# Performance work log

Hardware: AMD Instinct MI355X
Metric: run time of the kernel (lower is better)

## Reference

```python
import math
import jax, jax.numpy as jnp
import numpy as np

B, L, D, H = 2, 2048, 2048, 32
HD = D // H  # 64
ROPE_BASE = 10000.0


def _rope_tables():
    # standard RoPE: angles [L, HD/2], duplicated to [L, HD]
    inv_freq = 1.0 / (ROPE_BASE ** (np.arange(0, HD, 2, dtype=np.float32) / HD))
    t = np.arange(L, dtype=np.float32)
    ang = np.outer(t, inv_freq)                      # [L, HD/2]
    emb = np.concatenate([ang, ang], axis=-1)        # [L, HD]
    cos = np.broadcast_to(np.cos(emb), (B, L, HD)).copy()
    sin = np.broadcast_to(np.sin(emb), (B, L, HD)).copy()
    return jnp.asarray(cos), jnp.asarray(sin)


def setup_inputs() -> dict:
    key = jax.random.key(0)
    kx, kq, kp = jax.random.split(key, 3)
    x = jax.random.normal(kx, (B, L, D), dtype=jnp.float32)
    Wqkv = jax.random.normal(kq, (3 * D, D), dtype=jnp.float32) * 0.02
    Wproj = jax.random.normal(kp, (D, D), dtype=jnp.float32) * 0.02
    cos, sin = _rope_tables()
    return {"x": x, "cos": cos, "sin": sin, "Wqkv": Wqkv, "Wproj": Wproj}


def _rotate_half(t):
    t1, t2 = jnp.split(t, 2, axis=-1)
    return jnp.concatenate([-t2, t1], axis=-1)


def reference(x, cos, sin, Wqkv, Wproj):
    # fused QKV projection: [B,L,3D]
    qkv = jnp.einsum('bld,ed->ble', x, Wqkv)
    qkv = qkv.reshape(B, L, 3, H, HD).transpose(2, 0, 3, 1, 4)  # [3,B,H,L,HD]
    q, k, v = qkv[0], qkv[1], qkv[2]
    # RoPE (cos/sin broadcast over heads, matching cos.unsqueeze(1))
    c = cos[:, None, :, :]  # [B,1,L,HD]
    s = sin[:, None, :, :]
    q = q * c + _rotate_half(q) * s
    k = k * c + _rotate_half(k) * s
    # causal SDPA (L > 1 -> is_causal=True)
    scores = jnp.einsum('bhqd,bhkd->bhqk', q, k) / math.sqrt(HD)
    causal = jnp.tril(jnp.ones((L, L), dtype=bool))
    scores = jnp.where(causal, scores, jnp.float32(-1e30))
    attn = jax.nn.softmax(scores, axis=-1)
    y = jnp.einsum('bhqk,bhkd->bhqd', attn, v)
    y = y.transpose(0, 2, 1, 3).reshape(B, L, D)
    return jnp.einsum('bld,ed->ble', y, Wproj)
```

## Files before the change

### kernel.cpp

```cpp
#include <hip/hip_runtime.h>
#include <stdint.h>

#define DEV static __device__ __forceinline__

typedef __attribute__((ext_vector_type(8))) short bf16x8;
typedef __attribute__((ext_vector_type(4))) float f32x4;

DEV unsigned short f2b(float f){
  union { float f; unsigned int u; } v; v.f = f;
  return (unsigned short)((v.u + 0x7FFFu + ((v.u >> 16) & 1u)) >> 16);
}

#define SWZ(v, pat) __int_as_float(__builtin_amdgcn_ds_swizzle(__float_as_int(v), pat))

#define GLD16(g, l) __builtin_amdgcn_global_load_lds(                         \
    (const __attribute__((address_space(1))) void*)(g),                       \
    (__attribute__((address_space(3))) void*)(l), 16, 0, 0)

#define BAR() do { asm volatile("" ::: "memory"); __builtin_amdgcn_s_barrier(); \
                   asm volatile("" ::: "memory"); } while(0)

__global__ __launch_bounds__(256) void cvt_all(const float* __restrict__ a,
                                               const float* __restrict__ b,
                                               const float* __restrict__ c,
                                               unsigned short* __restrict__ oa,
                                               unsigned short* __restrict__ ob,
                                               unsigned short* __restrict__ oc){
  const int n1 = 2097152, n2 = 3145728, n3 = 1048576;
  int stride = gridDim.x * blockDim.x;
  for (int i = blockIdx.x * blockDim.x + threadIdx.x; i < n1 + n2 + n3; i += stride){
    const float* src; unsigned short* dst; int k;
    if (i < n1)            { src = a; dst = oa; k = i; }
    else if (i < n1 + n2)  { src = b; dst = ob; k = i - n1; }
    else                   { src = c; dst = oc; k = i - n1 - n2; }
    float4 v = ((const float4*)src)[k];
    ((ushort4*)dst)[k] = make_ushort4(f2b(v.x), f2b(v.y), f2b(v.z), f2b(v.w));
  }
}

template<int MODE>
__global__ __launch_bounds__(512, 2) void gemm_r3(
    const unsigned short* __restrict__ A,
    const unsigned short* __restrict__ Bw,
    int nbn,
    const float* __restrict__ cosp, const float* __restrict__ sinp,
    unsigned short* __restrict__ Qo, unsigned short* __restrict__ Ko,
    unsigned short* __restrict__ Vo, float* __restrict__ Cout, int N)
{
  constexpr int BUF = 49152;
  __shared__ __align__(16) unsigned char lds[3 * BUF];

  const int t = threadIdx.x;
  const int wid = t >> 6, lane = t & 63;
  const int l15 = lane & 15, l4 = lane >> 4;
  const int wr = wid >> 1, wc = wid & 1;

  const int cpx = gridDim.x >> 3;
  const int bid = (blockIdx.x & 7) * cpx + (blockIdx.x >> 3);
  const int bm = bid / nbn, bn = bid % nbn;
  const int m0 = bm * 256, n0 = bn * 128;

  const int rsub = lane >> 3;
  const int sch  = (lane & 7) ^ rsub;

  auto stage = [&](int kt, int rb){
    unsigned char* base = lds + rb * BUF;
    const unsigned short* As = A + (size_t)(m0 + wid * 32 + rsub) * 2048 + kt * 64 + sch * 8;
    #pragma unroll
    for (int i = 0; i < 4; ++i)
      GLD16(As + (size_t)i * 8 * 2048, base + wid * 4096 + i * 1024);
    #pragma unroll
    for (int j = 0; j < 2; ++j){
      int rv = n0 + wid * 16 + j * 8 + rsub;
      GLD16(Bw + (size_t)rv * 2048 + kt * 64 + sch * 8, base + 32768 + wid * 2048 + j * 1024);
    }
  };

  f32x4 acc[4][4];
  #pragma unroll
  for (int mi = 0; mi < 4; ++mi)
    #pragma unroll
    for (int ni = 0; ni < 4; ++ni)
      acc[mi][ni] = (f32x4){0.f, 0.f, 0.f, 0.f};

  auto compute = [&](int rb){
    const unsigned char* Ab = lds + rb * BUF;
    const unsigned char* Bb = Ab + 32768;
    bf16x8 af[4][2], bf[4][2];
    #pragma unroll
    for (int mi = 0; mi < 4; ++mi)
      #pragma unroll
      for (int ks = 0; ks < 2; ++ks){
        int r = wr * 64 + mi * 16 + l15, ch = ks * 4 + l4;
        af[mi][ks] = *(const bf16x8*)(Ab + r * 128 + ((ch * 16) ^ ((r & 7) << 4)));
      }
    #pragma unroll
    for (int ni = 0; ni < 4; ++ni)
      #pragma unroll
      for (int ks = 0; ks < 2; ++ks){
        int r = wc * 64 + ni * 16 + l15, ch = ks * 4 + l4;
        bf[ni][ks] = *(const bf16x8*)(Bb + r * 128 + ((ch * 16) ^ ((r & 7) << 4)));
      }
    #pragma unroll
    for (int ks = 0; ks < 2; ++ks)
      #pragma unroll
      for (int mi = 0; mi < 4; ++mi)
        #pragma unroll
        for (int ni = 0; ni < 4; ++ni)
          acc[mi][ni] = __builtin_amdgcn_mfma_f32_16x16x32_bf16(af[mi][ks], bf[ni][ks], acc[mi][ni], 0, 0, 0);
  };

  stage(0, 0);
  stage(1, 1);
  asm volatile("s_waitcnt vmcnt(6)" ::: "memory");
  __builtin_amdgcn_s_barrier();
  asm volatile("" ::: "memory");

  #pragma unroll 3
  for (int kt = 0; kt < 30; ++kt){
    stage(kt + 2, (kt + 2) % 3);
    asm volatile("s_waitcnt vmcnt(12)" ::: "memory");
    compute(kt % 3);
    asm volatile("" ::: "memory");
    __builtin_amdgcn_s_barrier();
    asm volatile("" ::: "memory");
  }
  asm volatile("s_waitcnt vmcnt(6)" ::: "memory");
  compute(0);
  asm volatile("" ::: "memory");
  __builtin_amdgcn_s_barrier();
  asm volatile("" ::: "memory");
  asm volatile("s_waitcnt vmcnt(0)" ::: "memory");
  compute(1);

  if (MODE == 1){
    #pragma unroll
    for (int mi = 0; mi < 4; ++mi)
      #pragma unroll
      for (int ni = 0; ni < 4; ++ni)
        #pragma unroll
        for (int j = 0; j < 4; ++j){
          int m = m0 + wr * 64 + mi * 16 + l4 * 4 + j;
          int n = n0 + wc * 64 + ni * 16 + l15;
          Cout[(size_t)m * N + n] = acc[mi][ni][j];
        }
  } else {
    #pragma unroll
    for (int ni = 0; ni < 4; ++ni){
      int e = n0 + wc * 64 + ni * 16 + l15;
      int which = e >> 11;
      int h = (e >> 6) & 31;
      int d = e & 63;
      unsigned short* dst = (which == 0) ? Qo : (which == 1) ? Ko : Vo;
      #pragma unroll
      for (int mi = 0; mi < 4; ++mi)
        #pragma unroll
        for (int j = 0; j < 4; ++j){
          int m = m0 + wr * 64 + mi * 16 + l4 * 4 + j;
          int b = m >> 11, l = m & 2047;
          float v = acc[mi][ni][j];
          float outv;
          if (which == 2){
            outv = v;
          } else {
            float pv = acc[mi][ni ^ 2][j];
            size_t ci = (size_t)(b * 2048 + l) * 64 + d;
            outv = v * cosp[ci] + ((d < 32) ? -pv : pv) * sinp[ci];
            if (which == 0) outv *= 0.125f;
          }
          dst[(size_t)((b * 32 + h) * 2048 + l) * 64 + d] = f2b(outv);
        }
    }
  }
}

__global__ __launch_bounds__(256) void transpose_v(const unsigned short* __restrict__ V,
                                                   unsigned short* __restrict__ Vt){
  __shared__ unsigned short tile[64][72];
  int bh = blockIdx.x >> 5;
  int l0 = (blockIdx.x & 31) * 64;
  int t = threadIdx.x;
  #pragma unroll
  for (int i = 0; i < 2; ++i){
    int c = i * 256 + t;
    int row = c >> 3, ch = c & 7;
    uint4 v = *(const uint4*)(V + ((size_t)bh * 2048 + l0 + row) * 64 + ch * 8);
    const unsigned short* p = (const unsigned short*)&v;
    #pragma unroll
    for (int k = 0; k < 8; ++k) tile[row][ch * 8 + k] = p[k];
  }
  __syncthreads();
  #pragma unroll
  for (int i = 0; i < 2; ++i){
    int c = i * 256 + t;
    int drow = c >> 3, ch = c & 7;
    unsigned short tmp[8];
    #pragma unroll
    for (int k = 0; k < 8; ++k) tmp[k] = tile[ch * 8 + k][drow];
    *(uint4*)(Vt + ((size_t)bh * 64 + drow) * 2048 + l0 + ch * 8) = *(const uint4*)tmp;
  }
}

__global__ __launch_bounds__(256, 3) void attn_fwd(
    const unsigned short* __restrict__ Q, const unsigned short* __restrict__ K,
    const unsigned short* __restrict__ Vt, unsigned short* __restrict__ Y)
{
  __shared__ __align__(16) unsigned char kvb[2][16384];
  __shared__ __align__(16) unsigned char plds[4][4096];
  int idx = blockIdx.x;
  int bh = idx >> 3;
  int pr = idx & 7;
  int b = bh >> 5, h = bh & 31;
  int t = threadIdx.x, wid = t >> 6, lane = t & 63;
  int l15 = lane & 15, l4 = lane >> 4;
  const unsigned short* Qb = Q  + (size_t)bh * 2048 * 64;
  const unsigned short* Kb = K  + (size_t)bh * 2048 * 64;
  const unsigned short* Vb = Vt + (size_t)bh * 64 * 2048;
  unsigned char* myp = plds[wid];

  int srow = t >> 3;
  int sch  = (t & 7) ^ (srow & 7);

  auto stageKV = [&](int kt, int ib){
    int kv0 = kt * 64;
    unsigned char* d = kvb[ib];
    GLD16(Kb + (size_t)(kv0 + srow)      * 64   + sch * 8, d + t * 16);
    GLD16(Kb + (size_t)(kv0 + srow + 32) * 64   + sch * 8, d + 4096  + t * 16);
    GLD16(Vb + (size_t)srow        * 2048 + kv0 + sch * 8, d + 8192  + t * 16);
    GLD16(Vb + (size_t)(srow + 32) * 2048 + kv0 + sch * 8, d + 12288 + t * 16);
  };

  for (int half = 0; half < 2; ++half){
    int qt = half ? (15 - pr) : pr;
    int q0 = qt * 128 + wid * 32;

    bf16x8 aq[2][2];
    #pragma unroll
    for (int mi = 0; mi < 2; ++mi)
      #pragma unroll
      for (int ks = 0; ks < 2; ++ks)
        aq[mi][ks] = *(const bf16x8*)(Qb + (size_t)(q0 + mi * 16 + l15) * 64 + ks * 32 + l4 * 8);

    f32x4 acc[2][4];
    float ps[2][4];
    #pragma unroll
    for (int mi = 0; mi < 2; ++mi){
      #pragma unroll
      for (int nd = 0; nd < 4; ++nd) acc[mi][nd] = (f32x4){0.f, 0.f, 0.f, 0.f};
      #pragma unroll
      for (int j = 0; j < 4; ++j) ps[mi][j] = 0.f;
    }

    int my_nkt = ((q0 + 31) >> 6) + 1;
    int nb = 2 * qt + 2;

    stageKV(0, 0);
    #pragma unroll 1
    for (int kt = 0; kt < nb; ++kt){
      int ib = kt & 1;
      if (kt + 1 < nb){
        stageKV(kt + 1, ib ^ 1);
        asm volatile("s_waitcnt vmcnt(4)" ::: "memory");
      } else {
        asm volatile("s_waitcnt vmcnt(0)" ::: "memory");
      }
      BAR();
      if (kt < my_nkt){
        const unsigned char* kb = kvb[ib];
        const unsigned char* vb = kvb[ib] + 8192;
        int kv0 = kt * 64;
        bf16x8 bk[2][4];
        #pragma unroll
        for (int ks = 0; ks < 2; ++ks)
          #pragma unroll
          for (int ni = 0; ni < 4; ++ni){
            int r = ni * 16 + l15, ch = ks * 4 + l4;
            bk[ks][ni] = *(const bf16x8*)(kb + r * 128 + ((ch * 16) ^ ((r & 7) << 4)));
          }
        f32x4 s[2][4];
        #pragma unroll
        for (int mi = 0; mi < 2; ++mi)
          #pragma unroll
          for (int ni = 0; ni < 4; ++ni)
            s[mi][ni] = (f32x4){0.f, 0.f, 0.f, 0.f};
        #pragma unroll
        for (int ks = 0; ks < 2; ++ks)
          #pragma unroll
          for (int mi = 0; mi < 2; ++mi)
            #pragma unroll
            for (int ni = 0; ni < 4; ++ni)
              s[mi][ni] = __builtin_amdgcn_mfma_f32_16x16x32_bf16(aq[mi][ks], bk[ks][ni], s[mi][ni], 0, 0, 0);
        if (kt == my_nkt - 1){
          #pragma unroll
          for (int mi = 0; mi < 2; ++mi)
            #pragma unroll
            for (int ni = 0; ni < 4; ++ni)
              #pragma unroll
              for (int j = 0; j < 4; ++j){
                int kv = kv0 + ni * 16 + l15;
                int q  = q0 + mi * 16 + l4 * 4 + j;
                if (kv > q) s[mi][ni][j] = -1e30f;
              }
        }
        #pragma unroll
        for (int mi = 0; mi < 2; ++mi)
          #pragma unroll
          for (int ni = 0; ni < 4; ++ni)
            #pragma unroll
            for (int j = 0; j < 4; ++j){
              float p = __expf(s[mi][ni][j]);
              s[mi][ni][j] = p;
              ps[mi][j] += p;
            }
        #pragma unroll
        for (int mi = 0; mi < 2; ++mi)
          #pragma unroll
          for (int j = 0; j < 4; ++j){
            int r = mi * 16 + l4 * 4 + j;
            int sw = (r & 7) << 4;
            unsigned char* rowp = myp + r * 128;
            #pragma unroll
            for (int p2 = 0; p2 < 2; ++p2){
              unsigned int pk;
              asm("v_cvt_pk_bf16_f32 %0, %1, %2" : "=v"(pk) : "v"(s[mi][2 * p2][j]), "v"(s[mi][2 * p2 + 1][j]));
              *(unsigned short*)(rowp + ((p2 * 64      + 2 * l15) ^ sw)) = (unsigned short)pk;
              *(unsigned short*)(rowp + ((p2 * 64 + 32 + 2 * l15) ^ sw)) = (unsigned short)(pk >> 16);
            }
          }
        __threadfence_block();
        #pragma unroll
        for (int ks2 = 0; ks2 < 2; ++ks2){
          bf16x8 ap[2], bv[4];
          #pragma unroll
          for (int mi = 0; mi < 2; ++mi){
            int r = mi * 16 + l15;
            ap[mi] = *(const bf16x8*)(myp + r * 128 + ((ks2 * 64 + l4 * 16) ^ ((r & 7) << 4)));
          }
          #pragma unroll
          for (int nd = 0; nd < 4; ++nd){
            int r = nd * 16 + l15, ch = ks2 * 4 + l4;
            bv[nd] = *(const bf16x8*)(vb + r * 128 + ((ch * 16) ^ ((r & 7) << 4)));
          }
          #pragma unroll
          for (int mi = 0; mi < 2; ++mi)
            #pragma unroll
            for (int nd = 0; nd < 4; ++nd)
              acc[mi][nd] = __builtin_amdgcn_mfma_f32_16x16x32_bf16(ap[mi], bv[nd], acc[mi][nd], 0, 0, 0);
        }
      }
      BAR();
    }

    float lrow[2][4];
    #pragma unroll
    for (int mi = 0; mi < 2; ++mi)
      #pragma unroll
      for (int j = 0; j < 4; ++j){
        float v = ps[mi][j];
        v += SWZ(v, 0x041F);
        v += SWZ(v, 0x081F);
        v += SWZ(v, 0x101F);
        v += SWZ(v, 0x201F);
        lrow[mi][j] = v;
      }
    #pragma unroll
    for (int mi = 0; mi < 2; ++mi){
      float inv[4];
      #pragma unroll
      for (int j = 0; j < 4; ++j) inv[j] = 1.f / lrow[mi][j];
      #pragma unroll
      for (int nd = 0; nd < 4; ++nd)
        #pragma unroll
        for (int j = 0; j < 4; ++j){
          int q = q0 + mi * 16 + l4 * 4 + j;
          int d = nd * 16 + l15;
          Y[(size_t)(b * 2048 + q) * 2048 + h * 64 + d] = f2b(acc[mi][nd][j] * inv[j]);
        }
    }
  }
}

extern "C" void kernel_launch(void* const* d_in, const int* in_sizes, int n_in,
                              void* d_out, int out_size, void* d_ws, size_t ws_size,
                              hipStream_t stream){
  (void)in_sizes; (void)n_in; (void)out_size; (void)ws_size;
  const float* x     = (const float*)d_in[0];
  const float* cosp  = (const float*)d_in[1];
  const float* sinp  = (const float*)d_in[2];
  const float* Wqkv  = (const float*)d_in[3];
  const float* Wproj = (const float*)d_in[4];
  float* out = (float*)d_out;
  char* ws = (char*)d_ws;

  unsigned short* Xb  = (unsigned short*)(ws);
  unsigned short* Wqb = (unsigned short*)(ws + 16777216);
  unsigned short* Wpb = (unsigned short*)(ws + 41943040);
  unsigned short* Qb  = (unsigned short*)(ws + 50331648);
  unsigned short* Kb  = (unsigned short*)(ws + 67108864);
  unsigned short* Vb  = (unsigned short*)(ws + 83886080);
  unsigned short* Vtb = Xb;
  unsigned short* Yb  = Vb;

  cvt_all<<<2048, 256, 0, stream>>>(x, Wqkv, Wproj, Xb, Wqb, Wpb);

  gemm_r3<0><<<768, 512, 0, stream>>>(Xb, Wqb, 48, cosp, sinp, Qb, Kb, Vb, nullptr, 0);
  transpose_v<<<2048, 256, 0, stream>>>(Vb, Vtb);
  attn_fwd<<<512, 256, 0, stream>>>(Qb, Kb, Vtb, Yb);
  gemm_r3<1><<<256, 512, 0, stream>>>(Yb, Wpb, 16, nullptr, nullptr, nullptr, nullptr, nullptr, out, 2048);
}
```

Baseline: 259.4 us.

## Add dedicated QKV GEMM with 256x192 tiles and interleaved RoPE row permutation

Replaces the templated QKV projection GEMM with a new kernel that uses 256x192 output tiles (512 blocks instead of 768), double-buffered LDS with staggered A/B staging, and an 8-way sub-phased MFMA schedule with barriers and setprio. The B rows are permuted so each RoPE pair lands in adjacent lanes, letting the epilogue fetch the partner value with a ds_swizzle instead of holding it in another accumulator tile. The aim is a larger tile with more reuse per LDS load and a better fit of blocks to CUs, at the cost of more LDS per block, many extra barriers and more complex indexing. The output projection keeps the old kernel minus the template.

```diff
diff --git a/kernel.cpp b/kernel.cpp
--- a/kernel.cpp
+++ b/kernel.cpp
@@ -38,14 +38,151 @@
   }
 }
 
-template<int MODE>
+__global__ __launch_bounds__(512, 2) void gemm_8p2(
+    const unsigned short* __restrict__ A,
+    const unsigned short* __restrict__ Bw,
+    const float* __restrict__ cosp, const float* __restrict__ sinp,
+    unsigned short* __restrict__ Qo, unsigned short* __restrict__ Ko,
+    unsigned short* __restrict__ Vo)
+{
+  constexpr int BUFSZ = 57344;
+  __shared__ __align__(16) unsigned char lds[2 * BUFSZ];
+  const int t = threadIdx.x;
+  const int wid = t >> 6, lane = t & 63;
+  const int l15 = lane & 15, l4 = lane >> 4;
+  const int wr = wid >> 2, wc = wid & 3;
+  const int nbn = 32;
+  const int cpx = gridDim.x >> 3;
+  const int bid = (blockIdx.x & 7) * cpx + (blockIdx.x >> 3);
+  const int bm = bid / nbn, bn = bid % nbn;
+  const int m0 = bm * 256, n0 = bn * 192;
+
+  const int tr  = t >> 3;
+  const int sch = (t & 7) ^ (tr & 7);
+  const int trp = (tr >> 1) | ((tr & 1) << 5);
+  const unsigned short* Abase = A  + (size_t)(m0 + tr)  * 2048 + sch * 8;
+  const unsigned short* Bbase = Bw + (size_t)(n0 + trp) * 2048 + sch * 8;
+
+  auto stageA = [&](int kt, int b){
+    size_t ko = (size_t)(kt & 31) * 64;
+    unsigned char* d = lds + b * BUFSZ + t * 16;
+    GLD16(Abase + ko,                      d);
+    GLD16(Abase + (size_t) 64 * 2048 + ko, d + 8192);
+    GLD16(Abase + (size_t)128 * 2048 + ko, d + 16384);
+    GLD16(Abase + (size_t)192 * 2048 + ko, d + 24576);
+  };
+  auto stageB = [&](int kt, int b){
+    size_t ko = (size_t)(kt & 31) * 64;
+    unsigned char* d = lds + b * BUFSZ + 32768 + t * 16;
+    GLD16(Bbase + ko,                      d);
+    GLD16(Bbase + (size_t) 64 * 2048 + ko, d + 8192);
+    GLD16(Bbase + (size_t)128 * 2048 + ko, d + 16384);
+  };
+
+  auto ldA = [&](bf16x8 (&af)[4], int b, int qm, int ks){
+    const unsigned char* Ar = lds + b * BUFSZ;
+    #pragma unroll
+    for (int mi = 0; mi < 4; ++mi){
+      int rr = wr * 128 + qm * 64 + mi * 16 + l15, ch = ks * 4 + l4;
+      af[mi] = *(const bf16x8*)(Ar + rr * 128 + ((ch * 16) ^ ((rr & 7) << 4)));
+    }
+  };
+  auto ldB = [&](bf16x8 (&bq)[3], int b, int ks){
+    const unsigned char* Br = lds + b * BUFSZ + 32768;
+    #pragma unroll
+    for (int ni = 0; ni < 3; ++ni){
+      int rr = wc * 48 + ni * 16 + l15, ch = ks * 4 + l4;
+      bq[ni] = *(const bf16x8*)(Br + rr * 128 + ((ch * 16) ^ ((rr & 7) << 4)));
+    }
+  };
+
+  f32x4 acc[8][3];
+  #pragma unroll
+  for (int mi = 0; mi < 8; ++mi)
+    #pragma unroll
+    for (int ni = 0; ni < 3; ++ni)
+      acc[mi][ni] = (f32x4){0.f, 0.f, 0.f, 0.f};
+
+#define MM3(AF, BQ, QM) do {                                                  \
+    __builtin_amdgcn_s_setprio(1);                                            \
+    _Pragma("unroll")                                                         \
+    for (int mi = 0; mi < 4; ++mi)                                            \
+      _Pragma("unroll")                                                       \
+      for (int ni = 0; ni < 3; ++ni)                                          \
+        acc[(QM)*4+mi][ni] = __builtin_amdgcn_mfma_f32_16x16x32_bf16(         \
+            (AF)[mi], (BQ)[ni], acc[(QM)*4+mi][ni], 0, 0, 0);                 \
+    __builtin_amdgcn_s_setprio(0);                                            \
+  } while (0)
+
+  stageA(0, 0); stageB(0, 0); stageB(1, 1);
+  asm volatile("s_waitcnt vmcnt(3)");
+  __builtin_amdgcn_s_barrier();
+
+  bf16x8 af[4], bq[3];
+  #pragma unroll 1
+  for (int T = 0; T < 32; ++T){
+    int b = T & 1;
+    ldA(af, b, 0, 0); ldB(bq, b, 0);
+    stageA(T + 1, b ^ 1);
+    __builtin_amdgcn_s_barrier();
+    asm volatile("s_waitcnt lgkmcnt(0)");
+    MM3(af, bq, 0);
+    __builtin_amdgcn_s_barrier();
+    ldA(af, b, 1, 0);
+    __builtin_amdgcn_s_barrier();
+    asm volatile("s_waitcnt lgkmcnt(0)");
+    MM3(af, bq, 1);
+    __builtin_amdgcn_s_barrier();
+    ldA(af, b, 0, 1); ldB(bq, b, 1);
+    __builtin_amdgcn_s_barrier();
+    asm volatile("s_waitcnt lgkmcnt(0)");
+    MM3(af, bq, 0);
+    __builtin_amdgcn_s_barrier();
+    ldA(af, b, 1, 1);
+    stageB(T + 2, b);
+    asm volatile("s_waitcnt vmcnt(3)");
+    __builtin_amdgcn_s_barrier();
+    asm volatile("s_waitcnt lgkmcnt(0)");
+    MM3(af, bq, 1);
+    __builtin_amdgcn_s_barrier();
+  }
+#undef MM3
+  asm volatile("s_waitcnt vmcnt(0)");
+  __builtin_amdgcn_s_barrier();
+
+  #pragma unroll
+  for (int ni = 0; ni < 3; ++ni){
+    int e16 = n0 + wc * 48 + ni * 16;
+    int which = e16 >> 11;
+    int h = (e16 >> 6) & 31;
+    unsigned short* dst = (which == 0) ? Qo : (which == 1) ? Ko : Vo;
+    int p = (e16 & 63) + l15;
+    int d = (p >> 1) | ((p & 1) << 5);
+    #pragma unroll
+    for (int mi = 0; mi < 8; ++mi)
+      #pragma unroll
+      for (int j = 0; j < 4; ++j){
+        int m = m0 + wr * 128 + mi * 16 + l4 * 4 + j;
+        int bb = m >> 11, l = m & 2047;
+        float val = acc[mi][ni][j];
+        float par = SWZ(val, 0x041F);
+        float outv;
+        if (which == 2){
+          outv = val;
+        } else {
+          size_t ci = (size_t)(bb * 2048 + l) * 64 + d;
+          outv = val * cosp[ci] + ((p & 1) ? par : -par) * sinp[ci];
+          if (which == 0) outv *= 0.125f;
+        }
+        dst[(size_t)((bb * 32 + h) * 2048 + l) * 64 + d] = f2b(outv);
+      }
+  }
+}
+
 __global__ __launch_bounds__(512, 2) void gemm_r3(
     const unsigned short* __restrict__ A,
     const unsigned short* __restrict__ Bw,
-    int nbn,
-    const float* __restrict__ cosp, const float* __restrict__ sinp,
-    unsigned short* __restrict__ Qo, unsigned short* __restrict__ Ko,
-    unsigned short* __restrict__ Vo, float* __restrict__ Cout, int N)
+    int nbn, float* __restrict__ Cout, int N)
 {
   constexpr int BUF = 49152;
   __shared__ __align__(16) unsigned char lds[3 * BUF];
@@ -133,45 +270,16 @@
   asm volatile("s_waitcnt vmcnt(0)" ::: "memory");
   compute(1);
 
-  if (MODE == 1){
-    #pragma unroll
-    for (int mi = 0; mi < 4; ++mi)
-      #pragma unroll
-      for (int ni = 0; ni < 4; ++ni)
-        #pragma unroll
-        for (int j = 0; j < 4; ++j){
-          int m = m0 + wr * 64 + mi * 16 + l4 * 4 + j;
-          int n = n0 + wc * 64 + ni * 16 + l15;
-          Cout[(size_t)m * N + n] = acc[mi][ni][j];
-        }
-  } else {
-    #pragma unroll
-    for (int ni = 0; ni < 4; ++ni){
-      int e = n0 + wc * 64 + ni * 16 + l15;
-      int which = e >> 11;
-      int h = (e >> 6) & 31;
-      int d = e & 63;
-      unsigned short* dst = (which == 0) ? Qo : (which == 1) ? Ko : Vo;
-      #pragma unroll
-      for (int mi = 0; mi < 4; ++mi)
-        #pragma unroll
-        for (int j = 0; j < 4; ++j){
-          int m = m0 + wr * 64 + mi * 16 + l4 * 4 + j;
-          int b = m >> 11, l = m & 2047;
-          float v = acc[mi][ni][j];
-          float outv;
-          if (which == 2){
-            outv = v;
-          } else {
-            float pv = acc[mi][ni ^ 2][j];
-            size_t ci = (size_t)(b * 2048 + l) * 64 + d;
-            outv = v * cosp[ci] + ((d < 32) ? -pv : pv) * sinp[ci];
-            if (which == 0) outv *= 0.125f;
-          }
-          dst[(size_t)((b * 32 + h) * 2048 + l) * 64 + d] = f2b(outv);
-        }
-    }
-  }
+  #pragma unroll
+  for (int mi = 0; mi < 4; ++mi)
+    #pragma unroll
+    for (int ni = 0; ni < 4; ++ni)
+      #pragma unroll
+      for (int j = 0; j < 4; ++j){
+        int m = m0 + wr * 64 + mi * 16 + l4 * 4 + j;
+        int n = n0 + wc * 64 + ni * 16 + l15;
+        Cout[(size_t)m * N + n] = acc[mi][ni][j];
+      }
 }
 
 __global__ __launch_bounds__(256) void transpose_v(const unsigned short* __restrict__ V,
@@ -403,8 +511,8 @@
 
   cvt_all<<<2048, 256, 0, stream>>>(x, Wqkv, Wproj, Xb, Wqb, Wpb);
 
-  gemm_r3<0><<<768, 512, 0, stream>>>(Xb, Wqb, 48, cosp, sinp, Qb, Kb, Vb, nullptr, 0);
+  gemm_8p2<<<512, 512, 0, stream>>>(Xb, Wqb, cosp, sinp, Qb, Kb, Vb);
   transpose_v<<<2048, 256, 0, stream>>>(Vb, Vtb);
   attn_fwd<<<512, 256, 0, stream>>>(Qb, Kb, Vtb, Yb);
-  gemm_r3<1><<<256, 512, 0, stream>>>(Yb, Wpb, 16, nullptr, nullptr, nullptr, nullptr, nullptr, out, 2048);
-}
+  gemm_r3<<<256, 512, 0, stream>>>(Yb, Wpb, 16, out, 2048);
+}
```

New measurement: 281.9 us. +8.7%, slower.
